# Optimization experiments

Hardware: AMD Instinct MI355X
Metric: run time of the kernel (lower is better)

## Reference

```python
import jax, jax.numpy as jnp
import numpy as np

EPS = 1e-08


def setup_inputs() -> dict:
    key = jax.random.key(0)
    k1, k2, k3 = jax.random.split(key, 3)
    B, T, IN, OUT = 32, 500, 2048, 1024
    x = jax.random.normal(k1, (B, T, IN), dtype=jnp.float32)
    # torch init: normal(mean=0, std=w_init_std*sqrt(1/input_shape))
    w = jax.random.normal(k2, (IN, OUT), dtype=jnp.float32) * np.sqrt(1.0 / IN)
    # b ~ N(1.0, 0.01), clamped >= 0
    b = jnp.clip(1.0 + 0.01 * jax.random.normal(k3, (OUT,), dtype=jnp.float32), 0.0, None)
    decay_m = jnp.array([0.6], dtype=jnp.float32)  # N(0.6, .01) clamped to [0,1]
    decay_s = jnp.array([0.9], dtype=jnp.float32)  # N(0.9, .01) clamped to [0,1]
    return {"x": x, "w": w, "b": b, "decay_m": decay_m, "decay_s": decay_s}


def reference(x, w, b, decay_m, decay_s):
    # x: [B, T, IN]; w: [IN, OUT]
    B, T, _ = x.shape
    OUT = w.shape[1]
    h = jnp.einsum('btc,cd->btd', x, w)          # [B, T, OUT]
    norm = jnp.sum(w * w, axis=0)                 # [OUT]
    dm = decay_m[0]
    ds = decay_s[0]
    inv_norm = 1.0 / (norm + EPS)
    zeros = jnp.zeros((B, OUT), dtype=x.dtype)
    # spk is never assigned a spike value in the original forward (spike_fn
    # is never applied), so it remains zero throughout.
    spk = zeros

    def step(carry, inp):
        M, S, E = carry
        E = dm * norm * (E + spk)                 # spk == 0 (faithful to source)
        M = dm * (M + inp)
        S = ds * (S + inp)
        mem = M - S - E
        mthr = mem * inv_norm - b                 # [B, OUT]
        return (M, S, E), mthr

    (_, _, _), spk_rec_t = jax.lax.scan(step, (zeros, zeros, zeros),
                                        jnp.swapaxes(h, 0, 1))  # [T, B, OUT]
    spk_rec = jnp.swapaxes(spk_rec_t, 0, 1)       # [B, T, OUT]
    loss = 0.5 * jnp.mean(spk_rec ** 2)
    return (spk_rec, loss)
```

## Files before the change

### kernel.cpp

```cpp
#include <hip/hip_runtime.h>


typedef __bf16 bf16x8 __attribute__((ext_vector_type(8)));
typedef __bf16 bf16x4 __attribute__((ext_vector_type(4)));
typedef float  f32x4  __attribute__((ext_vector_type(4)));

#define BDIM 32
#define TDIM 500
#define INDIM 2048
#define OUTDIM 1024
#define MROWS 16000
#define NCHUNK 25
#define CHLEN 20
#define OUT_ELEMS 16384000

__device__ __forceinline__ void gld_lds16(const void* g, void* l) {
    __builtin_amdgcn_global_load_lds(
        (const __attribute__((address_space(1))) unsigned int*)g,
        (__attribute__((address_space(3))) unsigned int*)l, 16, 0, 0);
}

__global__ void convert_x(const float* __restrict__ x, __bf16* __restrict__ xb) {
    size_t i = ((size_t)blockIdx.x * 256 + threadIdx.x) * 8;
    float4 a = *(const float4*)(x + i);
    float4 b = *(const float4*)(x + i + 4);
    bf16x8 o;
    o[0] = (__bf16)a.x; o[1] = (__bf16)a.y; o[2] = (__bf16)a.z; o[3] = (__bf16)a.w;
    o[4] = (__bf16)b.x; o[5] = (__bf16)b.y; o[6] = (__bf16)b.z; o[7] = (__bf16)b.w;
    *(bf16x8*)(xb + i) = o;
}

__global__ void transpose_w(const float* __restrict__ w, __bf16* __restrict__ wbt) {
    __shared__ float tile[32][33];
    const int tx = threadIdx.x;
    const int ty = threadIdx.y;
    const int d0 = blockIdx.x * 32;
    const int c0 = blockIdx.y * 32;
#pragma unroll
    for (int i = 0; i < 4; ++i) {
        int c = c0 + ty + i * 8;
        tile[ty + i * 8][tx] = w[(size_t)c * OUTDIM + d0 + tx];
    }
    __syncthreads();
#pragma unroll
    for (int i = 0; i < 4; ++i) {
        int d = d0 + ty + i * 8;
        wbt[(size_t)d * INDIM + c0 + tx] = (__bf16)tile[tx][ty + i * 8];
    }
}

__global__ void norm_w(const float* __restrict__ w, float* __restrict__ normAcc) {
    const int tid = threadIdx.x;
    const int c0 = blockIdx.x * 16;
    float acc0 = 0.f, acc1 = 0.f, acc2 = 0.f, acc3 = 0.f;
    for (int c = c0; c < c0 + 16; ++c) {
        const float* row = w + (size_t)c * OUTDIM;
        float v0 = row[tid];       acc0 += v0 * v0;
        float v1 = row[tid + 256]; acc1 += v1 * v1;
        float v2 = row[tid + 512]; acc2 += v2 * v2;
        float v3 = row[tid + 768]; acc3 += v3 * v3;
    }
    atomicAdd(&normAcc[tid], acc0);
    atomicAdd(&normAcc[tid + 256], acc1);
    atomicAdd(&normAcc[tid + 512], acc2);
    atomicAdd(&normAcc[tid + 768], acc3);
}

__global__ __launch_bounds__(256, 2) void gemm_bf16(
    const __bf16* __restrict__ A,
    const __bf16* __restrict__ Bt,
    __bf16* __restrict__ H)
{
    constexpr int K = INDIM;
    __shared__ __align__(16) __bf16 As[128 * 32];
    __shared__ __align__(16) __bf16 Bs[128 * 32];

    const int tid  = threadIdx.x;
    const int wave = tid >> 6;
    const int lane = tid & 63;
    const int bm = blockIdx.y * 128;
    const int bn = blockIdx.x * 128;
    const int wm = (wave & 1) * 64;
    const int wn = (wave >> 1) * 64;

    const int arow  = lane >> 2;
    const int aslot = lane & 3;
    const int quad = lane >> 4;
    const int mrow = lane & 15;
    const int fr   = ((mrow & 3) + ((mrow >> 2) & 3)) & 3;
    const int slot = ((quad + fr) & 3) * 8;

    f32x4 acc[4][4] = {};

    for (int k0 = 0; k0 < K; k0 += 32) {
        __syncthreads();
#pragma unroll
        for (int r = 0; r < 2; ++r) {
            const int rbase = r * 64 + wave * 16;
            const int row   = rbase + arow;
            const int f = ((row & 3) + ((row >> 2) & 3)) & 3;
            const int q = (aslot - f) & 3;
            gld_lds16(A  + (size_t)(bm + row) * K + (k0 + q * 8), &As[rbase * 32]);
            gld_lds16(Bt + (size_t)(bn + row) * K + (k0 + q * 8), &Bs[rbase * 32]);
        }
        __syncthreads();

        bf16x8 af[4], bfr[4];
#pragma unroll
        for (int i = 0; i < 4; ++i) {
            af[i]  = *(const bf16x8*)&As[(wm + i * 16 + mrow) * 32 + slot];
            bfr[i] = *(const bf16x8*)&Bs[(wn + i * 16 + mrow) * 32 + slot];
        }
#pragma unroll
        for (int i = 0; i < 4; ++i)
#pragma unroll
            for (int j = 0; j < 4; ++j)
                acc[i][j] = __builtin_amdgcn_mfma_f32_16x16x32_bf16(
                    af[i], bfr[j], acc[i][j], 0, 0, 0);
    }

#pragma unroll
    for (int i = 0; i < 4; ++i)
#pragma unroll
        for (int j = 0; j < 4; ++j)
#pragma unroll
            for (int r = 0; r < 4; ++r) {
                const int R = bm + wm + i * 16 + quad * 4 + r;
                const int C = bn + wn + j * 16 + mrow;
                H[(size_t)R * OUTDIM + C] = (__bf16)acc[i][j][r];
            }
}

__global__ void scan1(const __bf16* __restrict__ H,
                      f32x4* __restrict__ cM, f32x4* __restrict__ cS,
                      const float* __restrict__ dmp, const float* __restrict__ dsp) {
    const float dm = *dmp, ds = *dsp;
    const int c = blockIdx.x, b = blockIdx.y, tid = threadIdx.x;
    f32x4 M = {}, S = {};
    const __bf16* p = H + ((size_t)b * TDIM + c * CHLEN) * OUTDIM + tid * 4;
#pragma unroll 4
    for (int t = 0; t < CHLEN; ++t) {
        bf16x4 hv = *(const bf16x4*)(p + (size_t)t * OUTDIM);
        f32x4 h; h[0] = hv[0]; h[1] = hv[1]; h[2] = hv[2]; h[3] = hv[3];
        M = dm * (M + h);
        S = ds * (S + h);
    }
    const size_t idx = ((size_t)c * BDIM + b) * 256 + tid;
    cM[idx] = M;
    cS[idx] = S;
}

__global__ void scan2(f32x4* __restrict__ cM, f32x4* __restrict__ cS,
                      const float* __restrict__ dmp, const float* __restrict__ dsp) {
    const float dm = *dmp, ds = *dsp;
    float km = 1.f, ks = 1.f;
#pragma unroll
    for (int i = 0; i < CHLEN; ++i) { km *= dm; ks *= ds; }
    const int b = blockIdx.x, tid = threadIdx.x;
    f32x4 tM = {}, tS = {};
    for (int c = 0; c < NCHUNK; ++c) {
        const size_t idx = ((size_t)c * BDIM + b) * 256 + tid;
        f32x4 oM = cM[idx], oS = cS[idx];
        cM[idx] = tM; cS[idx] = tS;
        tM = km * tM + oM;
        tS = ks * tS + oS;
    }
}

__global__ void scan3(const __bf16* __restrict__ H,
                      const f32x4* __restrict__ cM, const f32x4* __restrict__ cS,
                      const float* __restrict__ normAcc, const float* __restrict__ bias,
                      const float* __restrict__ dmp, const float* __restrict__ dsp,
                      float* __restrict__ out, float* __restrict__ lossAcc) {
    const float dm = *dmp, ds = *dsp;
    const int c = blockIdx.x, b = blockIdx.y, tid = threadIdx.x;
    const size_t cidx = ((size_t)c * BDIM + b) * 256 + tid;
    f32x4 M = cM[cidx];
    f32x4 S = cS[cidx];
    f32x4 nv = *(const f32x4*)(normAcc + tid * 4);
    f32x4 inv;
    inv[0] = 1.f / (nv[0] + 1e-8f); inv[1] = 1.f / (nv[1] + 1e-8f);
    inv[2] = 1.f / (nv[2] + 1e-8f); inv[3] = 1.f / (nv[3] + 1e-8f);
    f32x4 bv = *(const f32x4*)(bias + tid * 4);

    const size_t rowbase = ((size_t)b * TDIM + c * CHLEN) * OUTDIM + tid * 4;
    const __bf16* p = H + rowbase;
    float* o = out + rowbase;
    float loss = 0.f;
#pragma unroll 4
    for (int t = 0; t < CHLEN; ++t) {
        bf16x4 hv = *(const bf16x4*)(p + (size_t)t * OUTDIM);
        f32x4 h; h[0] = hv[0]; h[1] = hv[1]; h[2] = hv[2]; h[3] = hv[3];
        M = dm * (M + h);
        S = ds * (S + h);
        f32x4 r = (M - S) * inv - bv;
        *(f32x4*)(o + (size_t)t * OUTDIM) = r;
        loss += r[0] * r[0] + r[1] * r[1] + r[2] * r[2] + r[3] * r[3];
    }
    __shared__ float red[256];
    red[tid] = loss;
    __syncthreads();
    for (int s = 128; s > 0; s >>= 1) {
        if (tid < s) red[tid] += red[tid + s];
        __syncthreads();
    }
    if (tid == 0) atomicAdd(lossAcc, red[0]);
}

__global__ void finalize(const float* __restrict__ lossAcc, float* __restrict__ out) {
    if (threadIdx.x == 0) out[OUT_ELEMS] = 0.5f * lossAcc[0] / (float)OUT_ELEMS;
}

#define OFF_H    ((size_t)0)
#define OFF_WBT  ((size_t)32768000)
#define OFF_NORM ((size_t)36962304)
#define OFF_LOSS ((size_t)36966400)
#define OFF_CM   ((size_t)36966656)
#define OFF_CS   ((size_t)40243456)

extern "C" void kernel_launch(void* const* d_in, const int* in_sizes, int n_in,
                              void* d_out, int out_size, void* d_ws, size_t ws_size,
                              hipStream_t stream) {
    const float* x  = (const float*)d_in[0];
    const float* w  = (const float*)d_in[1];
    const float* bb = (const float*)d_in[2];
    const float* dm = (const float*)d_in[3];
    const float* ds = (const float*)d_in[4];

    char* ws = (char*)d_ws;
    __bf16* H    = (__bf16*)(ws + OFF_H);
    __bf16* WBT  = (__bf16*)(ws + OFF_WBT);
    float*  NORM = (float*)(ws + OFF_NORM);
    float*  LOSS = (float*)(ws + OFF_LOSS);
    f32x4*  CM   = (f32x4*)(ws + OFF_CM);
    f32x4*  CS   = (f32x4*)(ws + OFF_CS);
    __bf16* XB   = (__bf16*)d_out;
    float*  out  = (float*)d_out;

    hipMemsetAsync(ws + OFF_NORM, 0, 4096 + 256, stream);

    convert_x<<<16000, 256, 0, stream>>>(x, XB);
    transpose_w<<<dim3(32, 64), dim3(32, 8), 0, stream>>>(w, WBT);
    norm_w<<<128, 256, 0, stream>>>(w, NORM);
    gemm_bf16<<<dim3(8, 125), 256, 0, stream>>>(XB, WBT, H);
    scan1<<<dim3(NCHUNK, BDIM), 256, 0, stream>>>(H, CM, CS, dm, ds);
    scan2<<<BDIM, 256, 0, stream>>>(CM, CS, dm, ds);
    scan3<<<dim3(NCHUNK, BDIM), 256, 0, stream>>>(H, CM, CS, NORM, bb, dm, ds, out, LOSS);
    finalize<<<1, 64, 0, stream>>>(LOSS, out);
}
```

Measured before the change: 351.4 us.

## Enlarge GEMM tile to 128x256 with K=64, fuse norm and loss finalize

```diff
diff --git a/kernel.cpp b/kernel.cpp
--- a/kernel.cpp
+++ b/kernel.cpp
@@ -30,40 +30,34 @@
     *(bf16x8*)(xb + i) = o;
 }
 
-__global__ void transpose_w(const float* __restrict__ w, __bf16* __restrict__ wbt) {
+__global__ void transpose_w(const float* __restrict__ w, __bf16* __restrict__ wbt,
+                            float* __restrict__ normAcc) {
     __shared__ float tile[32][33];
+    __shared__ float red[8][33];
     const int tx = threadIdx.x;
     const int ty = threadIdx.y;
     const int d0 = blockIdx.x * 32;
     const int c0 = blockIdx.y * 32;
+    float s = 0.f;
 #pragma unroll
     for (int i = 0; i < 4; ++i) {
         int c = c0 + ty + i * 8;
-        tile[ty + i * 8][tx] = w[(size_t)c * OUTDIM + d0 + tx];
-    }
+        float v = w[(size_t)c * OUTDIM + d0 + tx];
+        tile[ty + i * 8][tx] = v;
+        s += v * v;
+    }
+    red[ty][tx] = s;
     __syncthreads();
 #pragma unroll
     for (int i = 0; i < 4; ++i) {
         int d = d0 + ty + i * 8;
         wbt[(size_t)d * INDIM + c0 + tx] = (__bf16)tile[tx][ty + i * 8];
     }
-}
-
-__global__ void norm_w(const float* __restrict__ w, float* __restrict__ normAcc) {
-    const int tid = threadIdx.x;
-    const int c0 = blockIdx.x * 16;
-    float acc0 = 0.f, acc1 = 0.f, acc2 = 0.f, acc3 = 0.f;
-    for (int c = c0; c < c0 + 16; ++c) {
-        const float* row = w + (size_t)c * OUTDIM;
-        float v0 = row[tid];       acc0 += v0 * v0;
-        float v1 = row[tid + 256]; acc1 += v1 * v1;
-        float v2 = row[tid + 512]; acc2 += v2 * v2;
-        float v3 = row[tid + 768]; acc3 += v3 * v3;
-    }
-    atomicAdd(&normAcc[tid], acc0);
-    atomicAdd(&normAcc[tid + 256], acc1);
-    atomicAdd(&normAcc[tid + 512], acc2);
-    atomicAdd(&normAcc[tid + 768], acc3);
+    if (ty == 0) {
+        float t = red[0][tx] + red[1][tx] + red[2][tx] + red[3][tx]
+                + red[4][tx] + red[5][tx] + red[6][tx] + red[7][tx];
+        atomicAdd(&normAcc[d0 + tx], t);
+    }
 }
 
 __global__ __launch_bounds__(256, 2) void gemm_bf16(
@@ -72,60 +66,70 @@
     __bf16* __restrict__ H)
 {
     constexpr int K = INDIM;
-    __shared__ __align__(16) __bf16 As[128 * 32];
-    __shared__ __align__(16) __bf16 Bs[128 * 32];
+    __shared__ __align__(16) __bf16 As[128 * 64];
+    __shared__ __align__(16) __bf16 Bs[256 * 64];
 
     const int tid  = threadIdx.x;
     const int wave = tid >> 6;
     const int lane = tid & 63;
     const int bm = blockIdx.y * 128;
-    const int bn = blockIdx.x * 128;
-    const int wm = (wave & 1) * 64;
-    const int wn = (wave >> 1) * 64;
-
-    const int arow  = lane >> 2;
-    const int aslot = lane & 3;
+    const int bn = blockIdx.x * 256;
+    const int wn = wave * 64;
+
+    const int srow8 = lane >> 3;
+    const int sseg  = lane & 7;
     const int quad = lane >> 4;
     const int mrow = lane & 15;
-    const int fr   = ((mrow & 3) + ((mrow >> 2) & 3)) & 3;
-    const int slot = ((quad + fr) & 3) * 8;
-
-    f32x4 acc[4][4] = {};
-
-    for (int k0 = 0; k0 < K; k0 += 32) {
+
+    f32x4 acc[8][4] = {};
+
+    for (int k0 = 0; k0 < K; k0 += 64) {
         __syncthreads();
 #pragma unroll
-        for (int r = 0; r < 2; ++r) {
-            const int rbase = r * 64 + wave * 16;
-            const int row   = rbase + arow;
-            const int f = ((row & 3) + ((row >> 2) & 3)) & 3;
-            const int q = (aslot - f) & 3;
-            gld_lds16(A  + (size_t)(bm + row) * K + (k0 + q * 8), &As[rbase * 32]);
-            gld_lds16(Bt + (size_t)(bn + row) * K + (k0 + q * 8), &Bs[rbase * 32]);
+        for (int g = 0; g < 4; ++g) {
+            const int rbase = wave * 32 + g * 8;
+            const int row   = rbase + srow8;
+            const int q     = sseg ^ (row & 7);
+            gld_lds16(A + (size_t)(bm + row) * K + k0 + q * 8, &As[rbase * 64]);
+        }
+#pragma unroll
+        for (int g = 0; g < 8; ++g) {
+            const int rbase = wave * 64 + g * 8;
+            const int row   = rbase + srow8;
+            const int q     = sseg ^ (row & 7);
+            gld_lds16(Bt + (size_t)(bn + row) * K + k0 + q * 8, &Bs[rbase * 64]);
         }
         __syncthreads();
 
-        bf16x8 af[4], bfr[4];
-#pragma unroll
-        for (int i = 0; i < 4; ++i) {
-            af[i]  = *(const bf16x8*)&As[(wm + i * 16 + mrow) * 32 + slot];
-            bfr[i] = *(const bf16x8*)&Bs[(wn + i * 16 + mrow) * 32 + slot];
-        }
-#pragma unroll
-        for (int i = 0; i < 4; ++i)
-#pragma unroll
-            for (int j = 0; j < 4; ++j)
-                acc[i][j] = __builtin_amdgcn_mfma_f32_16x16x32_bf16(
-                    af[i], bfr[j], acc[i][j], 0, 0, 0);
-    }
-
-#pragma unroll
-    for (int i = 0; i < 4; ++i)
+#pragma unroll
+        for (int ks = 0; ks < 2; ++ks) {
+            bf16x8 af[8], bfr[4];
+#pragma unroll
+            for (int i = 0; i < 8; ++i) {
+                const int r = i * 16 + mrow;
+                af[i] = *(const bf16x8*)&As[r * 64 + (((ks * 4 + quad) ^ (r & 7)) * 8)];
+            }
+#pragma unroll
+            for (int j = 0; j < 4; ++j) {
+                const int r = wn + j * 16 + mrow;
+                bfr[j] = *(const bf16x8*)&Bs[r * 64 + (((ks * 4 + quad) ^ (r & 7)) * 8)];
+            }
+#pragma unroll
+            for (int i = 0; i < 8; ++i)
+#pragma unroll
+                for (int j = 0; j < 4; ++j)
+                    acc[i][j] = __builtin_amdgcn_mfma_f32_16x16x32_bf16(
+                        af[i], bfr[j], acc[i][j], 0, 0, 0);
+        }
+    }
+
+#pragma unroll
+    for (int i = 0; i < 8; ++i)
 #pragma unroll
         for (int j = 0; j < 4; ++j)
 #pragma unroll
             for (int r = 0; r < 4; ++r) {
-                const int R = bm + wm + i * 16 + quad * 4 + r;
+                const int R = bm + i * 16 + quad * 4 + r;
                 const int C = bn + wn + j * 16 + mrow;
                 H[(size_t)R * OUTDIM + C] = (__bf16)acc[i][j][r];
             }
@@ -150,17 +154,18 @@
     cS[idx] = S;
 }
 
-__global__ void scan2(f32x4* __restrict__ cM, f32x4* __restrict__ cS,
+__global__ void scan2(float* __restrict__ cM, float* __restrict__ cS,
                       const float* __restrict__ dmp, const float* __restrict__ dsp) {
     const float dm = *dmp, ds = *dsp;
     float km = 1.f, ks = 1.f;
 #pragma unroll
     for (int i = 0; i < CHLEN; ++i) { km *= dm; ks *= ds; }
-    const int b = blockIdx.x, tid = threadIdx.x;
-    f32x4 tM = {}, tS = {};
+    const int gid = blockIdx.x * 256 + threadIdx.x;
+    const int b = gid >> 10, d = gid & 1023;
+    float tM = 0.f, tS = 0.f;
     for (int c = 0; c < NCHUNK; ++c) {
-        const size_t idx = ((size_t)c * BDIM + b) * 256 + tid;
-        f32x4 oM = cM[idx], oS = cS[idx];
+        const size_t idx = (((size_t)c * BDIM + b) << 10) + d;
+        float oM = cM[idx], oS = cS[idx];
         cM[idx] = tM; cS[idx] = tS;
         tM = km * tM + oM;
         tS = ks * tS + oS;
@@ -171,7 +176,8 @@
                       const f32x4* __restrict__ cM, const f32x4* __restrict__ cS,
                       const float* __restrict__ normAcc, const float* __restrict__ bias,
                       const float* __restrict__ dmp, const float* __restrict__ dsp,
-                      float* __restrict__ out, float* __restrict__ lossAcc) {
+                      float* __restrict__ out, float* __restrict__ lossAcc,
+                      unsigned* __restrict__ ticket) {
     const float dm = *dmp, ds = *dsp;
     const int c = blockIdx.x, b = blockIdx.y, tid = threadIdx.x;
     const size_t cidx = ((size_t)c * BDIM + b) * 256 + tid;
@@ -204,19 +210,24 @@
         if (tid < s) red[tid] += red[tid + s];
         __syncthreads();
     }
-    if (tid == 0) atomicAdd(lossAcc, red[0]);
-}
-
-__global__ void finalize(const float* __restrict__ lossAcc, float* __restrict__ out) {
-    if (threadIdx.x == 0) out[OUT_ELEMS] = 0.5f * lossAcc[0] / (float)OUT_ELEMS;
-}
-
-#define OFF_H    ((size_t)0)
-#define OFF_WBT  ((size_t)32768000)
-#define OFF_NORM ((size_t)36962304)
-#define OFF_LOSS ((size_t)36966400)
-#define OFF_CM   ((size_t)36966656)
-#define OFF_CS   ((size_t)40243456)
+    if (tid == 0) {
+        atomicAdd(lossAcc, red[0]);
+        __threadfence();
+        unsigned t = atomicAdd(ticket, 1u);
+        if (t == NCHUNK * BDIM - 1) {
+            float total = atomicAdd(lossAcc, 0.0f);
+            out[OUT_ELEMS] = 0.5f * total / (float)OUT_ELEMS;
+        }
+    }
+}
+
+#define OFF_H      ((size_t)0)
+#define OFF_WBT    ((size_t)32768000)
+#define OFF_NORM   ((size_t)36962304)
+#define OFF_LOSS   ((size_t)36966400)
+#define OFF_TICKET ((size_t)36966404)
+#define OFF_CM     ((size_t)36966656)
+#define OFF_CS     ((size_t)40243456)
 
 extern "C" void kernel_launch(void* const* d_in, const int* in_sizes, int n_in,
                               void* d_out, int out_size, void* d_ws, size_t ws_size,
@@ -228,23 +239,23 @@
     const float* ds = (const float*)d_in[4];
 
     char* ws = (char*)d_ws;
-    __bf16* H    = (__bf16*)(ws + OFF_H);
-    __bf16* WBT  = (__bf16*)(ws + OFF_WBT);
-    float*  NORM = (float*)(ws + OFF_NORM);
-    float*  LOSS = (float*)(ws + OFF_LOSS);
-    f32x4*  CM   = (f32x4*)(ws + OFF_CM);
-    f32x4*  CS   = (f32x4*)(ws + OFF_CS);
-    __bf16* XB   = (__bf16*)d_out;
-    float*  out  = (float*)d_out;
+    __bf16*   H    = (__bf16*)(ws + OFF_H);
+    __bf16*   WBT  = (__bf16*)(ws + OFF_WBT);
+    float*    NORM = (float*)(ws + OFF_NORM);
+    float*    LOSS = (float*)(ws + OFF_LOSS);
+    unsigned* TICK = (unsigned*)(ws + OFF_TICKET);
+    f32x4*    CM   = (f32x4*)(ws + OFF_CM);
+    f32x4*    CS   = (f32x4*)(ws + OFF_CS);
+    __bf16*   XB   = (__bf16*)d_out;
+    float*    out  = (float*)d_out;
 
     hipMemsetAsync(ws + OFF_NORM, 0, 4096 + 256, stream);
 
     convert_x<<<16000, 256, 0, stream>>>(x, XB);
-    transpose_w<<<dim3(32, 64), dim3(32, 8), 0, stream>>>(w, WBT);
-    norm_w<<<128, 256, 0, stream>>>(w, NORM);
-    gemm_bf16<<<dim3(8, 125), 256, 0, stream>>>(XB, WBT, H);
+    transpose_w<<<dim3(32, 64), dim3(32, 8), 0, stream>>>(w, WBT, NORM);
+    gemm_bf16<<<dim3(4, 125), 256, 0, stream>>>(XB, WBT, H);
     scan1<<<dim3(NCHUNK, BDIM), 256, 0, stream>>>(H, CM, CS, dm, ds);
-    scan2<<<BDIM, 256, 0, stream>>>(CM, CS, dm, ds);
-    scan3<<<dim3(NCHUNK, BDIM), 256, 0, stream>>>(H, CM, CS, NORM, bb, dm, ds, out, LOSS);
-    finalize<<<1, 64, 0, stream>>>(LOSS, out);
-}
+    scan2<<<128, 256, 0, stream>>>((float*)CM, (float*)CS, dm, ds);
+    scan3<<<dim3(NCHUNK, BDIM), 256, 0, stream>>>(H, CM, CS, NORM, bb, dm, ds,
+                                                  out, LOSS, TICK);
+}
```

Measured after the change: 335.0 us. 4.7% less time.
